# Kernel tuning notes

Hardware: AMD Instinct MI355X
Metric: run time of the kernel (lower is better)

## Reference

```python
import jax, jax.numpy as jnp
import numpy as np

HIDDEN = 1024
HEADS = 16
HEAD_DIM = HIDDEN // HEADS
EPS = 1e-6


def _layernorm(x, gamma, beta):
    mu = jnp.mean(x, axis=-1, keepdims=True)
    var = jnp.mean(jnp.square(x - mu), axis=-1, keepdims=True)
    return (x - mu) * jax.lax.rsqrt(var + EPS) * gamma + beta


def setup_inputs() -> dict:
    key = jax.random.key(0)
    ks = jax.random.split(key, 16)
    B, S, D = 2, 2048, HIDDEN
    s = 1.0 / np.sqrt(D)
    inp = {
        "x": jax.random.normal(ks[0], (B, S, D), dtype=jnp.float32),
        "Wq": jax.random.uniform(ks[1], (D, D), jnp.float32, -s, s),
        "bq": jnp.zeros((D,), jnp.float32),
        "Wk": jax.random.uniform(ks[2], (D, D), jnp.float32, -s, s),
        "bk": jnp.zeros((D,), jnp.float32),
        "Wv": jax.random.uniform(ks[3], (D, D), jnp.float32, -s, s),
        "bv": jnp.zeros((D,), jnp.float32),
        "Wo": jax.random.uniform(ks[4], (D, D), jnp.float32, -s, s),
        "bo": jnp.zeros((D,), jnp.float32),
        "g1": jnp.ones((D,), jnp.float32),
        "b1": jnp.zeros((D,), jnp.float32),
        "Wup": jax.random.uniform(ks[5], (D, 4 * D), jnp.float32, -s, s),
        "bup": jnp.zeros((4 * D,), jnp.float32),
        "Wdn": jax.random.uniform(ks[6], (4 * D, D), jnp.float32, -0.5 * s, 0.5 * s),
        "bdn": jnp.zeros((D,), jnp.float32),
        "g2": jnp.ones((D,), jnp.float32),
        "b2": jnp.zeros((D,), jnp.float32),
    }
    return inp


def _forward(x, Wq, bq, Wk, bk, Wv, bv, Wo, bo, g1, b1, Wup, bup, Wdn, bdn, g2, b2):
    B, S, D = x.shape
    H, Hd = HEADS, HEAD_DIM
    # projections -> (B, H, S, Hd)
    q = (x @ Wq + bq).reshape(B, S, H, Hd).transpose(0, 2, 1, 3)
    k = (x @ Wk + bk).reshape(B, S, H, Hd).transpose(0, 2, 1, 3)
    v = (x @ Wv + bv).reshape(B, S, H, Hd).transpose(0, 2, 1, 3)
    # full NxN scores (faithful to the source: explicit QK^T, mask, softmax, AV)
    scores = jnp.einsum("bhqd,bhkd->bhqk", q, k) / np.sqrt(Hd)
    causal = jnp.tril(jnp.ones((S, S), dtype=bool))  # (S, S)
    scores = jnp.where(causal, scores, jnp.float32(-1e20))
    attn = jax.nn.softmax(scores, axis=-1)
    # dropout is identity in eval mode
    mid = jnp.einsum("bhqk,bhkd->bqhd", attn, v).reshape(B, S, D)
    attn_out = mid @ Wo + bo
    x = _layernorm(x + attn_out, g1, b1)
    # FFN
    up = jax.nn.relu(x @ Wup + bup)
    down = up @ Wdn + bdn
    return _layernorm(x + down, g2, b2)


def reference(x, Wq, bq, Wk, bk, Wv, bv, Wo, bo, g1, b1, Wup, bup, Wdn, bdn, g2, b2):
    return _forward(x, Wq, bq, Wk, bk, Wv, bv, Wo, bo, g1, b1, Wup, bup, Wdn, bdn, g2, b2)
```

## Files before the change

### kernel.cpp

```cpp
#include <hip/hip_runtime.h>

#define D_MODEL 1024
#define D_FFN   4096
#define SEQ     2048
#define NROWS   4096
#define QKV_LD  3072

typedef __bf16 bf16x8 __attribute__((ext_vector_type(8)));
typedef float  floatx4 __attribute__((ext_vector_type(4)));

#define MFMA_BF16 __builtin_amdgcn_mfma_f32_16x16x32_bf16

__device__ __forceinline__ unsigned short f2bf(float f) {
  unsigned int u = __float_as_uint(f);
  u += 0x7FFFu + ((u >> 16) & 1u);
  return (unsigned short)(u >> 16);
}

template <int C>
__device__ __forceinline__ float ror16(float x) {
  return __int_as_float(
      __builtin_amdgcn_mov_dpp(__float_as_int(x), 0x120 | C, 0xf, 0xf, true));
}

__device__ __forceinline__ void async16(const unsigned short* g, unsigned short* l) {
  __builtin_amdgcn_global_load_lds(
      (const __attribute__((address_space(1))) unsigned int*)g,
      (__attribute__((address_space(3))) unsigned int*)l, 16, 0, 0);
}

__global__ __launch_bounds__(256) void k_f32_to_bf16(
    const float* __restrict__ in, unsigned short* __restrict__ outp, long n) {
  long i = ((long)blockIdx.x * 256 + threadIdx.x) * 4;
  if (i >= n) return;
  float4 v = *(const float4*)(in + i);
  ushort4 o;
  o.x = f2bf(v.x); o.y = f2bf(v.y); o.z = f2bf(v.z); o.w = f2bf(v.w);
  *(ushort4*)(outp + i) = o;
}

__global__ __launch_bounds__(256) void k_transpose_bf16(
    const float* __restrict__ W, unsigned short* __restrict__ WT, int R, int C) {
  __shared__ float tile[32][33];
  int tx = threadIdx.x & 31, ty = threadIdx.x >> 5;
  long bx = (long)blockIdx.x * 32;
  long by = (long)blockIdx.y * 32;
  #pragma unroll
  for (int j = 0; j < 4; j++)
    tile[ty + j * 8][tx] = W[(by + ty + j * 8) * C + bx + tx];
  __syncthreads();
  #pragma unroll
  for (int j = 0; j < 4; j++)
    WT[(bx + ty + j * 8) * R + by + tx] = f2bf(tile[tx][ty + j * 8]);
}

__global__ __launch_bounds__(256) void k_transpose_sq(
    const float* __restrict__ Wq, const float* __restrict__ Wk,
    const float* __restrict__ Wv, const float* __restrict__ Wo,
    unsigned short* __restrict__ WqkvT, unsigned short* __restrict__ WoT) {
  __shared__ float tile[32][33];
  int z = blockIdx.z;
  const float* W = (z == 0) ? Wq : (z == 1) ? Wk : (z == 2) ? Wv : Wo;
  unsigned short* dst = (z < 3) ? (WqkvT + (size_t)z * D_MODEL * D_MODEL) : WoT;
  int tx = threadIdx.x & 31, ty = threadIdx.x >> 5;
  long bx = (long)blockIdx.x * 32;
  long by = (long)blockIdx.y * 32;
  #pragma unroll
  for (int j = 0; j < 4; j++)
    tile[ty + j * 8][tx] = W[(by + ty + j * 8) * D_MODEL + bx + tx];
  __syncthreads();
  #pragma unroll
  for (int j = 0; j < 4; j++)
    dst[(bx + ty + j * 8) * D_MODEL + by + tx] = f2bf(tile[tx][ty + j * 8]);
}

__global__ __launch_bounds__(256) void k_pack_bias(
    const float* __restrict__ bq, const float* __restrict__ bk,
    const float* __restrict__ bv, float* __restrict__ dst) {
  int i = blockIdx.x * 256 + threadIdx.x;
  if (i >= 3072) return;
  float v = (i < 1024) ? bq[i] : (i < 2048) ? bk[i - 1024] : bv[i - 2048];
  dst[i] = v;
}

__global__ __launch_bounds__(256) void k_transpose_v(
    const unsigned short* __restrict__ QKV, unsigned short* __restrict__ Vt) {
  __shared__ unsigned short tile[64][72];
  int r0 = blockIdx.x * 64;
  int c0 = blockIdx.y * 64;
  int tx = threadIdx.x & 15, ty = threadIdx.x >> 4;
  #pragma unroll
  for (int j = 0; j < 4; j++) {
    int r = ty + j * 16;
    *(ushort4*)&tile[r][tx * 4] =
        *(const ushort4*)(QKV + (long)(r0 + r) * QKV_LD + 2048 + c0 + tx * 4);
  }
  __syncthreads();
  #pragma unroll
  for (int j = 0; j < 4; j++) {
    int d = ty + j * 16;
    ushort4 o;
    o.x = tile[tx * 4 + 0][d];
    o.y = tile[tx * 4 + 1][d];
    o.z = tile[tx * 4 + 2][d];
    o.w = tile[tx * 4 + 3][d];
    *(ushort4*)(Vt + (long)(c0 + d) * NROWS + r0 + tx * 4) = o;
  }
}

__global__ __launch_bounds__(512, 2) void k_gemm256(
    const unsigned short* __restrict__ A,
    const unsigned short* __restrict__ Bt,
    const float* __restrict__ bias,
    void* __restrict__ Cp, int M, int N, int K, int flags) {
  extern __shared__ unsigned short lds[];
  int tid = threadIdx.x, lane = tid & 63, wave = tid >> 6;
  int quad = lane >> 4, l16 = lane & 15;
  int wm = wave >> 2, wn = wave & 3;

  int nwg = gridDim.x * gridDim.y;
  int orig = blockIdx.y * gridDim.x + blockIdx.x;
  int wg = (orig & 7) * (nwg >> 3) + (orig >> 3);
  long bm = (long)(wg & 15) * 256;
  long bn = (long)(wg >> 4) * 256;

  int z = blockIdx.z;
  int Ks = K / gridDim.z;
  long zb = (long)z * Ks;
  int T = Ks / 64;

  const floatx4 fz = {0.f, 0.f, 0.f, 0.f};
  floatx4 acc[8][4];
  #pragma unroll
  for (int i = 0; i < 8; i++)
    #pragma unroll
    for (int j = 0; j < 4; j++) acc[i][j] = fz;

  int srow = tid >> 3;
  int sc = (tid & 7) ^ (srow & 7);
  const unsigned short* Ag = A + (bm + srow) * (long)K + zb + sc * 8;
  const unsigned short* Bg = Bt + (bn + srow) * (long)K + zb + sc * 8;

  auto stage = [&](int tt, int c) {
    unsigned short* An = lds + c * 32768;
    unsigned short* Bn = An + 16384;
    long ko = (long)tt * 64;
    #pragma unroll
    for (int i = 0; i < 4; i++) {
      async16(Ag + (long)i * 64 * K + ko, An + i * 4096 + wave * 512);
      async16(Bg + (long)i * 64 * K + ko, Bn + i * 4096 + wave * 512);
    }
  };

  int aoff = (wm * 128 + l16) * 64;
  int boff = (wn * 64 + l16) * 64;
  int sw = l16 & 7;
  int ca0 = (quad ^ sw) * 8;
  int ca1 = ((4 + quad) ^ sw) * 8;

  stage(0, 0);
  for (int t = 0; t < T; t++) {
    int c = t & 1;
    const unsigned short* Ac = lds + c * 32768;
    const unsigned short* Bc = Ac + 16384;
    int tn = (t + 1 < T) ? t + 1 : T - 1;
    stage(tn, c ^ 1);
    __asm__ volatile("s_waitcnt vmcnt(8)" ::: "memory");
    __builtin_amdgcn_s_barrier();

    bf16x8 af[8], b0, b1;
    #pragma unroll
    for (int m = 0; m < 8; m++) af[m] = *(const bf16x8*)(Ac + aoff + m * 1024 + ca0);
    b0 = *(const bf16x8*)(Bc + boff + 0 * 1024 + ca0);
    b1 = *(const bf16x8*)(Bc + boff + 1 * 1024 + ca0);
    __asm__ volatile("s_waitcnt lgkmcnt(0)" ::: "memory");
    __builtin_amdgcn_s_setprio(1);
    #pragma unroll
    for (int m = 0; m < 8; m++) acc[m][0] = MFMA_BF16(af[m], b0, acc[m][0], 0, 0, 0);
    #pragma unroll
    for (int m = 0; m < 8; m++) acc[m][1] = MFMA_BF16(af[m], b1, acc[m][1], 0, 0, 0);
    __builtin_amdgcn_s_setprio(0);
    __builtin_amdgcn_s_barrier();
    b0 = *(const bf16x8*)(Bc + boff + 2 * 1024 + ca0);
    b1 = *(const bf16x8*)(Bc + boff + 3 * 1024 + ca0);
    __asm__ volatile("s_waitcnt lgkmcnt(0)" ::: "memory");
    __builtin_amdgcn_s_setprio(1);
    #pragma unroll
    for (int m = 0; m < 8; m++) acc[m][2] = MFMA_BF16(af[m], b0, acc[m][2], 0, 0, 0);
    #pragma unroll
    for (int m = 0; m < 8; m++) acc[m][3] = MFMA_BF16(af[m], b1, acc[m][3], 0, 0, 0);
    __builtin_amdgcn_s_setprio(0);
    __builtin_amdgcn_s_barrier();
    #pragma unroll
    for (int m = 0; m < 8; m++) af[m] = *(const bf16x8*)(Ac + aoff + m * 1024 + ca1);
    b0 = *(const bf16x8*)(Bc + boff + 0 * 1024 + ca1);
    b1 = *(const bf16x8*)(Bc + boff + 1 * 1024 + ca1);
    __asm__ volatile("s_waitcnt lgkmcnt(0)" ::: "memory");
    __builtin_amdgcn_s_setprio(1);
    #pragma unroll
    for (int m = 0; m < 8; m++) acc[m][0] = MFMA_BF16(af[m], b0, acc[m][0], 0, 0, 0);
    #pragma unroll
    for (int m = 0; m < 8; m++) acc[m][1] = MFMA_BF16(af[m], b1, acc[m][1], 0, 0, 0);
    __builtin_amdgcn_s_setprio(0);
    __builtin_amdgcn_s_barrier();
    b0 = *(const bf16x8*)(Bc + boff + 2 * 1024 + ca1);
    b1 = *(const bf16x8*)(Bc + boff + 3 * 1024 + ca1);
    __asm__ volatile("s_waitcnt lgkmcnt(0)" ::: "memory");
    __builtin_amdgcn_s_setprio(1);
    #pragma unroll
    for (int m = 0; m < 8; m++) acc[m][2] = MFMA_BF16(af[m], b0, acc[m][2], 0, 0, 0);
    #pragma unroll
    for (int m = 0; m < 8; m++) acc[m][3] = MFMA_BF16(af[m], b1, acc[m][3], 0, 0, 0);
    __builtin_amdgcn_s_setprio(0);
    __builtin_amdgcn_s_barrier();
  }

  bool f32out = (flags & 1) != 0;
  bool relu   = (flags & 2) != 0;
  float* outf = (float*)Cp + (size_t)z * M * (size_t)N;
  unsigned short* outh = (unsigned short*)Cp;
  #pragma unroll
  for (int n = 0; n < 4; n++) {
    long col = bn + wn * 64 + n * 16 + l16;
    float bvv = (z == 0) ? bias[col] : 0.0f;
    #pragma unroll
    for (int m = 0; m < 8; m++) {
      long row = bm + wm * 128 + m * 16 + quad * 4;
      #pragma unroll
      for (int r = 0; r < 4; r++) {
        float v = acc[m][n][r] + bvv;
        if (relu) v = fmaxf(v, 0.0f);
        if (f32out) outf[(row + r) * (long)N + col] = v;
        else        outh[(row + r) * (long)N + col] = f2bf(v);
      }
    }
  }
}

#define PLD 72
__global__ __launch_bounds__(256) void k_attn(
    const unsigned short* __restrict__ QKV,
    const unsigned short* __restrict__ Vt,
    unsigned short* __restrict__ Omat) {
  __shared__ unsigned short Ks[64 * 64];
  __shared__ unsigned short Vs[64 * 64];
  __shared__ unsigned short Ps[4][16 * PLD];
  int tid = threadIdx.x;
  int lane = tid & 63, wave = tid >> 6;
  int quad = lane >> 4, l16 = lane & 15;
  int z = blockIdx.x;
  int bh = z & 31;
  int qp = z >> 5;
  int b = bh >> 4, h = bh & 15;
  long rowbase = (long)b * SEQ;
  int hd0 = h * 64;
  unsigned short* pw = &Ps[wave][0];
  const float SCL = 0.18033688f;
  const floatx4 fz = {0.f, 0.f, 0.f, 0.f};

  int r_in = lane >> 3;
  int cpos = lane & 7;

  bf16x8 ones;
  #pragma unroll
  for (int i = 0; i < 8; i++) ones[i] = (__bf16)1.0f;

  #pragma unroll
  for (int phase = 0; phase < 2; phase++) {
    int qt = phase ? qp : (31 - qp);
    int q0w = qt * 64 + wave * 16;
    int qrow = q0w + quad * 4;
    int ntiles = qt + 1;

    bf16x8 qf0, qf1;
    {
      const unsigned short* qp_ =
          QKV + (rowbase + q0w + l16) * (long)QKV_LD + hd0 + quad * 8;
      qf0 = *(const bf16x8*)(qp_);
      qf1 = *(const bf16x8*)(qp_ + 32);
    }

    floatx4 ao[4], aol;
    #pragma unroll
    for (int t = 0; t < 4; t++) ao[t] = fz;
    aol = fz;
    float m_i[4];
    #pragma unroll
    for (int r = 0; r < 4; r++) m_i[r] = -3.0e38f;

    for (int it = 0; it < ntiles; it++) {
      int kv0 = it << 6;
      #pragma unroll
      for (int jj = 0; jj < 2; jj++) {
        int j = wave * 2 + jj;
        int r = j * 8 + r_in;
        int c = cpos ^ (r & 7);
        const unsigned short* gk =
            QKV + (rowbase + kv0 + r) * (long)QKV_LD + 1024 + hd0 + c * 8;
        async16(gk, Ks + j * 512);
        const unsigned short* gv =
            Vt + (long)(hd0 + r) * NROWS + rowbase + kv0 + c * 8;
        async16(gv, Vs + j * 512);
      }
      __syncthreads();

      floatx4 sacc[4];
      #pragma unroll
      for (int t = 0; t < 4; t++) {
        int row = t * 16 + l16;
        int sw = row & 7;
        bf16x8 kf0 = *(const bf16x8*)(Ks + row * 64 + (quad ^ sw) * 8);
        bf16x8 kf1 = *(const bf16x8*)(Ks + row * 64 + ((quad + 4) ^ sw) * 8);
        sacc[t] = __builtin_amdgcn_mfma_f32_16x16x32_bf16(qf0, kf0, fz, 0, 0, 0);
        sacc[t] = __builtin_amdgcn_mfma_f32_16x16x32_bf16(qf1, kf1, sacc[t], 0, 0, 0);
      }

      bool maskt = (it == ntiles - 1);
      if (maskt) {
        #pragma unroll
        for (int t = 0; t < 4; t++) {
          int kvc = kv0 + t * 16 + l16;
          #pragma unroll
          for (int r = 0; r < 4; r++) {
            float s = sacc[t][r] * SCL;
            sacc[t][r] = (kvc > qrow + r) ? -1.0e30f : s;
          }
        }
      } else {
        #pragma unroll
        for (int t = 0; t < 4; t++)
          #pragma unroll
          for (int r = 0; r < 4; r++) sacc[t][r] *= SCL;
      }

      float Mg = sacc[0][0];
      #pragma unroll
      for (int t = 0; t < 4; t++)
        #pragma unroll
        for (int r = 0; r < 4; r++) Mg = fmaxf(Mg, sacc[t][r]);
      Mg = fmaxf(Mg, ror16<1>(Mg));
      Mg = fmaxf(Mg, ror16<2>(Mg));
      Mg = fmaxf(Mg, ror16<4>(Mg));
      Mg = fmaxf(Mg, ror16<8>(Mg));

      float alpha[4];
      #pragma unroll
      for (int r = 0; r < 4; r++) {
        float mn = fmaxf(m_i[r], Mg);
        alpha[r] = __builtin_amdgcn_exp2f(m_i[r] - mn);
        m_i[r] = mn;
      }

      #pragma unroll
      for (int t = 0; t < 4; t++)
        #pragma unroll
        for (int r = 0; r < 4; r++) {
          float p = __builtin_amdgcn_exp2f(sacc[t][r] - m_i[r]);
          pw[(quad * 4 + r) * PLD + t * 16 + l16] =
              (unsigned short)(__float_as_uint(p) >> 16);
        }

      #pragma unroll
      for (int t = 0; t < 4; t++)
        #pragma unroll
        for (int r = 0; r < 4; r++) ao[t][r] *= alpha[r];
      #pragma unroll
      for (int r = 0; r < 4; r++) aol[r] *= alpha[r];

      __asm__ volatile("s_waitcnt lgkmcnt(0)" ::: "memory");
      bf16x8 pf0 = *(const bf16x8*)(pw + l16 * PLD + quad * 8);
      bf16x8 pf1 = *(const bf16x8*)(pw + l16 * PLD + 32 + quad * 8);

      #pragma unroll
      for (int t = 0; t < 4; t++) {
        int row = t * 16 + l16;
        int sw = row & 7;
        bf16x8 vf0 = *(const bf16x8*)(Vs + row * 64 + (quad ^ sw) * 8);
        bf16x8 vf1 = *(const bf16x8*)(Vs + row * 64 + ((quad + 4) ^ sw) * 8);
        ao[t] = __builtin_amdgcn_mfma_f32_16x16x32_bf16(pf0, vf0, ao[t], 0, 0, 0);
        ao[t] = __builtin_amdgcn_mfma_f32_16x16x32_bf16(pf1, vf1, ao[t], 0, 0, 0);
      }
      aol = __builtin_amdgcn_mfma_f32_16x16x32_bf16(pf0, ones, aol, 0, 0, 0);
      aol = __builtin_amdgcn_mfma_f32_16x16x32_bf16(pf1, ones, aol, 0, 0, 0);

      __syncthreads();
    }

    float inv[4];
    #pragma unroll
    for (int r = 0; r < 4; r++) inv[r] = 1.0f / aol[r];
    #pragma unroll
    for (int t = 0; t < 4; t++)
      #pragma unroll
      for (int r = 0; r < 4; r++)
        Omat[(rowbase + qrow + r) * (long)D_MODEL + hd0 + t * 16 + l16] =
            f2bf(ao[t][r] * inv[r]);
  }
}

__global__ __launch_bounds__(256) void k_add_ln(
    const float* __restrict__ A, const float* __restrict__ P,
    const float* __restrict__ g, const float* __restrict__ be,
    float* __restrict__ Y, unsigned short* __restrict__ Ybf) {
  __shared__ float sb[4], ssb[4];
  const long PS = (long)NROWS * D_MODEL;
  int tid = threadIdx.x;
  long base = (long)blockIdx.x * D_MODEL + tid * 4;
  float4 a  = *(const float4*)(A + base);
  float4 p0 = *(const float4*)(P + base);
  float4 p1 = *(const float4*)(P + PS + base);
  float4 p2 = *(const float4*)(P + 2 * PS + base);
  float4 p3 = *(const float4*)(P + 3 * PS + base);
  float v0 = a.x + p0.x + p1.x + p2.x + p3.x;
  float v1 = a.y + p0.y + p1.y + p2.y + p3.y;
  float v2 = a.z + p0.z + p1.z + p2.z + p3.z;
  float v3 = a.w + p0.w + p1.w + p2.w + p3.w;
  float s  = v0 + v1 + v2 + v3;
  float ss = v0 * v0 + v1 * v1 + v2 * v2 + v3 * v3;
  #pragma unroll
  for (int o = 32; o >= 1; o >>= 1) {
    s  += __shfl_xor(s, o, 64);
    ss += __shfl_xor(ss, o, 64);
  }
  int wave = tid >> 6;
  if ((tid & 63) == 0) { sb[wave] = s; ssb[wave] = ss; }
  __syncthreads();
  s  = sb[0] + sb[1] + sb[2] + sb[3];
  ss = ssb[0] + ssb[1] + ssb[2] + ssb[3];
  float mu  = s * (1.0f / 1024.0f);
  float var = ss * (1.0f / 1024.0f) - mu * mu;
  float rstd = rsqrtf(var + 1e-6f);
  float4 gv  = *(const float4*)(g + tid * 4);
  float4 bev = *(const float4*)(be + tid * 4);
  float o0 = (v0 - mu) * rstd * gv.x + bev.x;
  float o1 = (v1 - mu) * rstd * gv.y + bev.y;
  float o2 = (v2 - mu) * rstd * gv.z + bev.z;
  float o3 = (v3 - mu) * rstd * gv.w + bev.w;
  if (Y) *(float4*)(Y + base) = make_float4(o0, o1, o2, o3);
  if (Ybf) {
    ushort4 u;
    u.x = f2bf(o0); u.y = f2bf(o1); u.z = f2bf(o2); u.w = f2bf(o3);
    *(ushort4*)(Ybf + base) = u;
  }
}

extern "C" void kernel_launch(void* const* d_in, const int* in_sizes, int n_in,
                              void* d_out, int out_size, void* d_ws, size_t ws_size,
                              hipStream_t stream) {
  (void)in_sizes; (void)n_in; (void)out_size; (void)ws_size;
  static bool s_attr = false;
  if (!s_attr) {
    hipFuncSetAttribute((const void*)k_gemm256,
                        hipFuncAttributeMaxDynamicSharedMemorySize, 131072);
    s_attr = true;
  }
  const float* x   = (const float*)d_in[0];
  const float* Wq  = (const float*)d_in[1];
  const float* bq  = (const float*)d_in[2];
  const float* Wk  = (const float*)d_in[3];
  const float* bk  = (const float*)d_in[4];
  const float* Wv  = (const float*)d_in[5];
  const float* bv  = (const float*)d_in[6];
  const float* Wo  = (const float*)d_in[7];
  const float* bo  = (const float*)d_in[8];
  const float* g1  = (const float*)d_in[9];
  const float* b1  = (const float*)d_in[10];
  const float* Wup = (const float*)d_in[11];
  const float* bup = (const float*)d_in[12];
  const float* Wdn = (const float*)d_in[13];
  const float* bdn = (const float*)d_in[14];
  const float* g2  = (const float*)d_in[15];
  const float* b2  = (const float*)d_in[16];
  float* out = (float*)d_out;

  char* ws = (char*)d_ws;
  size_t off = 0;
  auto alloc = [&](size_t bytes) {
    char* p = ws + off;
    off = (off + bytes + 255) & ~(size_t)255;
    return p;
  };
  unsigned short* x_bf   = (unsigned short*)alloc((size_t)NROWS * D_MODEL * 2);
  unsigned short* WqkvT  = (unsigned short*)alloc((size_t)QKV_LD * D_MODEL * 2);
  unsigned short* WoT    = (unsigned short*)alloc((size_t)D_MODEL * D_MODEL * 2);
  unsigned short* WupT   = (unsigned short*)alloc((size_t)D_FFN * D_MODEL * 2);
  unsigned short* WdnT   = (unsigned short*)alloc((size_t)D_MODEL * D_FFN * 2);
  float*          bqkv   = (float*)alloc((size_t)QKV_LD * 4);
  unsigned short* qkv_bf = (unsigned short*)alloc((size_t)NROWS * QKV_LD * 2);
  unsigned short* Vt     = (unsigned short*)alloc((size_t)D_MODEL * NROWS * 2);
  unsigned short* mid_bf = (unsigned short*)alloc((size_t)NROWS * D_MODEL * 2);
  float*          x1f    = (float*)alloc((size_t)NROWS * D_MODEL * 4);
  unsigned short* x1bf   = (unsigned short*)alloc((size_t)NROWS * D_MODEL * 2);
  float*          part   = (float*)alloc((size_t)4 * NROWS * D_MODEL * 4);
  unsigned short* h_bf   = (unsigned short*)alloc((size_t)NROWS * D_FFN * 2);

  k_f32_to_bf16<<<4096, 256, 0, stream>>>(x, x_bf, (long)NROWS * D_MODEL);
  k_transpose_sq<<<dim3(32, 32, 4), 256, 0, stream>>>(Wq, Wk, Wv, Wo, WqkvT, WoT);
  k_transpose_bf16<<<dim3(128, 32), 256, 0, stream>>>(Wup, WupT, D_MODEL, D_FFN);
  k_transpose_bf16<<<dim3(32, 128), 256, 0, stream>>>(Wdn, WdnT, D_FFN, D_MODEL);
  k_pack_bias<<<12, 256, 0, stream>>>(bq, bk, bv, bqkv);

  k_gemm256<<<dim3(16, 12, 1), 512, 131072, stream>>>(x_bf, WqkvT, bqkv, qkv_bf,
                                                      NROWS, QKV_LD, D_MODEL, 0);
  k_transpose_v<<<dim3(64, 16), 256, 0, stream>>>(qkv_bf, Vt);

  k_attn<<<512, 256, 0, stream>>>(qkv_bf, Vt, mid_bf);

  k_gemm256<<<dim3(16, 4, 4), 512, 131072, stream>>>(mid_bf, WoT, bo, part,
                                                     NROWS, D_MODEL, D_MODEL, 1);
  k_add_ln<<<4096, 256, 0, stream>>>(x, part, g1, b1, x1f, x1bf);

  k_gemm256<<<dim3(16, 16, 1), 512, 131072, stream>>>(x1bf, WupT, bup, h_bf,
                                                      NROWS, D_FFN, D_MODEL, 2);
  k_gemm256<<<dim3(16, 4, 4), 512, 131072, stream>>>(h_bf, WdnT, bdn, part,
                                                     NROWS, D_MODEL, D_FFN, 1);
  k_add_ln<<<4096, 256, 0, stream>>>(x1f, part, g2, b2, out, nullptr);
}
```

Before: 388.7 us.

## Add 128x128 GEMM kernel and drop split-K partials for narrow GEMMs

Adds a 128x128-tile bf16 MFMA GEMM with double-buffered async LDS staging and uses it for the QKV, output-projection and down-projection GEMMs. The N=1024 GEMMs no longer use four-way split-K, so the partial buffer shrinks to one slice and the add+layernorm reads a single partial instead of four. This is meant to raise workgroup count and occupancy on the smaller GEMMs and cut partial-sum memory traffic. The cost is less data reuse per tile and, for the down projection, a long K=4096 loop per block that split-K used to spread across more blocks.

```diff
diff --git a/kernel.cpp b/kernel.cpp
--- a/kernel.cpp
+++ b/kernel.cpp
@@ -105,6 +105,109 @@
     o.z = tile[tx * 4 + 2][d];
     o.w = tile[tx * 4 + 3][d];
     *(ushort4*)(Vt + (long)(c0 + d) * NROWS + r0 + tx * 4) = o;
+  }
+}
+
+__global__ __launch_bounds__(512, 4) void k_gemm128(
+    const unsigned short* __restrict__ A,
+    const unsigned short* __restrict__ Bt,
+    const float* __restrict__ bias,
+    void* __restrict__ Cp, int M, int N, int K, int flags) {
+  __shared__ unsigned short lds[2 * 16384];
+  int tid = threadIdx.x, lane = tid & 63, wave = tid >> 6;
+  int quad = lane >> 4, l16 = lane & 15;
+  int wm = wave >> 2, wn = wave & 3;
+
+  int gx = gridDim.x;
+  int nwg = gx * gridDim.y;
+  int orig = blockIdx.y * gx + blockIdx.x;
+  int wg = (orig & 7) * (nwg >> 3) + (orig >> 3);
+  long bm = (long)(wg % gx) * 128;
+  long bn = (long)(wg / gx) * 128;
+
+  int T = K / 64;
+
+  const floatx4 fz = {0.f, 0.f, 0.f, 0.f};
+  floatx4 acc[4][2];
+  #pragma unroll
+  for (int i = 0; i < 4; i++)
+    #pragma unroll
+    for (int j = 0; j < 2; j++) acc[i][j] = fz;
+
+  int srow = tid >> 3;
+  int sc = (tid & 7) ^ (srow & 7);
+  const unsigned short* Ag = A + (bm + srow) * (long)K + sc * 8;
+  const unsigned short* Bg = Bt + (bn + srow) * (long)K + sc * 8;
+
+  auto stage = [&](int tt, int c) {
+    unsigned short* An = lds + c * 16384;
+    unsigned short* Bn = An + 8192;
+    long ko = (long)tt * 64;
+    async16(Ag + ko, An + wave * 512);
+    async16(Ag + 64 * (long)K + ko, An + 4096 + wave * 512);
+    async16(Bg + ko, Bn + wave * 512);
+    async16(Bg + 64 * (long)K + ko, Bn + 4096 + wave * 512);
+  };
+
+  int aoff = (wm * 64 + l16) * 64;
+  int boff = (wn * 32 + l16) * 64;
+  int sw = l16 & 7;
+  int ca0 = (quad ^ sw) * 8;
+  int ca1 = ((4 + quad) ^ sw) * 8;
+
+  stage(0, 0);
+  for (int t = 0; t < T; t++) {
+    int c = t & 1;
+    const unsigned short* Ac = lds + c * 16384;
+    const unsigned short* Bc = Ac + 8192;
+    int tn = (t + 1 < T) ? t + 1 : T - 1;
+    stage(tn, c ^ 1);
+    __asm__ volatile("s_waitcnt vmcnt(4)" ::: "memory");
+    __builtin_amdgcn_s_barrier();
+
+    bf16x8 af[4][2], bfr[2][2];
+    #pragma unroll
+    for (int m = 0; m < 4; m++) {
+      af[m][0] = *(const bf16x8*)(Ac + aoff + m * 1024 + ca0);
+      af[m][1] = *(const bf16x8*)(Ac + aoff + m * 1024 + ca1);
+    }
+    #pragma unroll
+    for (int n = 0; n < 2; n++) {
+      bfr[n][0] = *(const bf16x8*)(Bc + boff + n * 1024 + ca0);
+      bfr[n][1] = *(const bf16x8*)(Bc + boff + n * 1024 + ca1);
+    }
+    __asm__ volatile("s_waitcnt lgkmcnt(0)" ::: "memory");
+    __builtin_amdgcn_s_setprio(1);
+    #pragma unroll
+    for (int h = 0; h < 2; h++)
+      #pragma unroll
+      for (int m = 0; m < 4; m++)
+        #pragma unroll
+        for (int n = 0; n < 2; n++)
+          acc[m][n] = MFMA_BF16(af[m][h], bfr[n][h], acc[m][n], 0, 0, 0);
+    __builtin_amdgcn_s_setprio(0);
+    __builtin_amdgcn_s_barrier();
+  }
+
+  bool f32out = (flags & 1) != 0;
+  bool relu   = (flags & 2) != 0;
+  float* outf = (float*)Cp;
+  unsigned short* outh = (unsigned short*)Cp;
+  #pragma unroll
+  for (int n = 0; n < 2; n++) {
+    long col = bn + wn * 32 + n * 16 + l16;
+    float bvv = bias[col];
+    #pragma unroll
+    for (int m = 0; m < 4; m++) {
+      long row = bm + wm * 64 + m * 16 + quad * 4;
+      #pragma unroll
+      for (int r = 0; r < 4; r++) {
+        float v = acc[m][n][r] + bvv;
+        if (relu) v = fmaxf(v, 0.0f);
+        if (f32out) outf[(row + r) * (long)N + col] = v;
+        else        outh[(row + r) * (long)N + col] = f2bf(v);
+      }
+    }
   }
 }
 
@@ -403,18 +506,14 @@
     const float* __restrict__ g, const float* __restrict__ be,
     float* __restrict__ Y, unsigned short* __restrict__ Ybf) {
   __shared__ float sb[4], ssb[4];
-  const long PS = (long)NROWS * D_MODEL;
   int tid = threadIdx.x;
   long base = (long)blockIdx.x * D_MODEL + tid * 4;
   float4 a  = *(const float4*)(A + base);
   float4 p0 = *(const float4*)(P + base);
-  float4 p1 = *(const float4*)(P + PS + base);
-  float4 p2 = *(const float4*)(P + 2 * PS + base);
-  float4 p3 = *(const float4*)(P + 3 * PS + base);
-  float v0 = a.x + p0.x + p1.x + p2.x + p3.x;
-  float v1 = a.y + p0.y + p1.y + p2.y + p3.y;
-  float v2 = a.z + p0.z + p1.z + p2.z + p3.z;
-  float v3 = a.w + p0.w + p1.w + p2.w + p3.w;
+  float v0 = a.x + p0.x;
+  float v1 = a.y + p0.y;
+  float v2 = a.z + p0.z;
+  float v3 = a.w + p0.w;
   float s  = v0 + v1 + v2 + v3;
   float ss = v0 * v0 + v1 * v1 + v2 * v2 + v3 * v3;
   #pragma unroll
@@ -491,7 +590,7 @@
   unsigned short* mid_bf = (unsigned short*)alloc((size_t)NROWS * D_MODEL * 2);
   float*          x1f    = (float*)alloc((size_t)NROWS * D_MODEL * 4);
   unsigned short* x1bf   = (unsigned short*)alloc((size_t)NROWS * D_MODEL * 2);
-  float*          part   = (float*)alloc((size_t)4 * NROWS * D_MODEL * 4);
+  float*          part   = (float*)alloc((size_t)NROWS * D_MODEL * 4);
   unsigned short* h_bf   = (unsigned short*)alloc((size_t)NROWS * D_FFN * 2);
 
   k_f32_to_bf16<<<4096, 256, 0, stream>>>(x, x_bf, (long)NROWS * D_MODEL);
@@ -500,19 +599,19 @@
   k_transpose_bf16<<<dim3(32, 128), 256, 0, stream>>>(Wdn, WdnT, D_FFN, D_MODEL);
   k_pack_bias<<<12, 256, 0, stream>>>(bq, bk, bv, bqkv);
 
-  k_gemm256<<<dim3(16, 12, 1), 512, 131072, stream>>>(x_bf, WqkvT, bqkv, qkv_bf,
-                                                      NROWS, QKV_LD, D_MODEL, 0);
+  k_gemm128<<<dim3(32, 24), 512, 0, stream>>>(x_bf, WqkvT, bqkv, qkv_bf,
+                                              NROWS, QKV_LD, D_MODEL, 0);
   k_transpose_v<<<dim3(64, 16), 256, 0, stream>>>(qkv_bf, Vt);
 
   k_attn<<<512, 256, 0, stream>>>(qkv_bf, Vt, mid_bf);
 
-  k_gemm256<<<dim3(16, 4, 4), 512, 131072, stream>>>(mid_bf, WoT, bo, part,
-                                                     NROWS, D_MODEL, D_MODEL, 1);
+  k_gemm128<<<dim3(32, 8), 512, 0, stream>>>(mid_bf, WoT, bo, part,
+                                             NROWS, D_MODEL, D_MODEL, 1);
   k_add_ln<<<4096, 256, 0, stream>>>(x, part, g1, b1, x1f, x1bf);
 
   k_gemm256<<<dim3(16, 16, 1), 512, 131072, stream>>>(x1bf, WupT, bup, h_bf,
                                                       NROWS, D_FFN, D_MODEL, 2);
-  k_gemm256<<<dim3(16, 4, 4), 512, 131072, stream>>>(h_bf, WdnT, bdn, part,
-                                                     NROWS, D_MODEL, D_FFN, 1);
+  k_gemm128<<<dim3(32, 8), 512, 0, stream>>>(h_bf, WdnT, bdn, part,
+                                             NROWS, D_MODEL, D_FFN, 1);
   k_add_ln<<<4096, 256, 0, stream>>>(x1f, part, g2, b2, out, nullptr);
 }
```

Measured after the change: 363.2 us. -6.6%, faster.
